# Optimization experiments

Measured on AMD Instinct MI355X. Metric: run time of the kernel, lower is better.

The kernel has to match this reference:

```python
import jax, jax.numpy as jnp
import numpy as np

T = 200                      # TRAIN_ROIS_PER_IMAGE
RATIO = 0.33                 # ROI_POSITIVE_RATIO
P_MAX = int(T * RATIO)       # max positive ROIs (66)
MH, MW = 28, 28              # MASK_SHAPE
STD = jnp.array([0.1, 0.1, 0.2, 0.2], jnp.float32)  # BBOX_STD_DEV
EPS = 1e-6


def _iou(a, b):
    # a [N,4], b [G,4] -> [N,G] IoU (same math as overlaps_graph, without tiling)
    ay1, ax1, ay2, ax2 = a[:, 0:1], a[:, 1:2], a[:, 2:3], a[:, 3:4]
    by1, bx1, by2, bx2 = b[None, :, 0], b[None, :, 1], b[None, :, 2], b[None, :, 3]
    iy = jnp.maximum(jnp.minimum(ay2, by2) - jnp.maximum(ay1, by1), 0.0)
    ix = jnp.maximum(jnp.minimum(ax2, bx2) - jnp.maximum(ax1, bx1), 0.0)
    inter = iy * ix
    union = (ay2 - ay1) * (ax2 - ax1) + (by2 - by1) * (bx2 - bx1) - inter
    return inter / jnp.maximum(union, EPS)


def _box_refinement(box, gt):
    # standard Mask R-CNN box_refinement_graph
    h = jnp.maximum(box[:, 2] - box[:, 0], EPS)
    w = jnp.maximum(box[:, 3] - box[:, 1], EPS)
    cy = box[:, 0] + 0.5 * h
    cx = box[:, 1] + 0.5 * w
    gh = jnp.maximum(gt[:, 2] - gt[:, 0], EPS)
    gw = jnp.maximum(gt[:, 3] - gt[:, 1], EPS)
    gcy = gt[:, 0] + 0.5 * gh
    gcx = gt[:, 1] + 0.5 * gw
    return jnp.stack([(gcy - cy) / h, (gcx - cx) / w,
                      jnp.log(gh / h), jnp.log(gw / w)], axis=-1)


def _crop_and_resize(imgs, boxes):
    # imgs [T,H,W], boxes [T,4] normalized; TF crop_and_resize bilinear semantics,
    # extrapolation_value = 0 for samples outside [0, H-1] x [0, W-1].
    Tn, H, W = imgs.shape
    y1, x1, y2, x2 = boxes[:, 0], boxes[:, 1], boxes[:, 2], boxes[:, 3]
    iy = jnp.arange(MH, dtype=jnp.float32)
    ix = jnp.arange(MW, dtype=jnp.float32)
    ys = y1[:, None] * (H - 1) + iy[None, :] * ((y2 - y1) * (H - 1) / (MH - 1))[:, None]  # [T,MH]
    xs = x1[:, None] * (W - 1) + ix[None, :] * ((x2 - x1) * (W - 1) / (MW - 1))[:, None]  # [T,MW]
    y0 = jnp.floor(ys); x0 = jnp.floor(xs)
    wy = (ys - y0)[:, :, None]
    wx = (xs - x0)[:, None, :]
    y0i = jnp.clip(y0, 0, H - 1).astype(jnp.int32)
    y1i = jnp.clip(y0 + 1, 0, H - 1).astype(jnp.int32)
    x0i = jnp.clip(x0, 0, W - 1).astype(jnp.int32)
    x1i = jnp.clip(x0 + 1, 0, W - 1).astype(jnp.int32)
    t = jnp.arange(Tn)[:, None, None]
    v00 = imgs[t, y0i[:, :, None], x0i[:, None, :]]
    v01 = imgs[t, y0i[:, :, None], x1i[:, None, :]]
    v10 = imgs[t, y1i[:, :, None], x0i[:, None, :]]
    v11 = imgs[t, y1i[:, :, None], x1i[:, None, :]]
    val = (v00 * (1 - wx) + v01 * wx) * (1 - wy) + (v10 * (1 - wx) + v11 * wx) * wy
    ok = ((ys >= 0) & (ys <= H - 1))[:, :, None] & ((xs >= 0) & (xs <= W - 1))[:, None, :]
    return jnp.where(ok, val, 0.0)


def _targets_one(proposals, class_ids, boxes, masks):
    # proposals [N,4], class_ids [G] int, boxes [G,4], masks [H,W,G]
    N = proposals.shape[0]
    # zero-padding trim expressed as validity masks (jit-friendly fixed shapes)
    valid_prop = jnp.any(proposals != 0, axis=1)
    valid_gt = jnp.any(boxes != 0, axis=1)
    non_crowd = (class_ids > 0) & valid_gt
    crowd = (class_ids < 0) & valid_gt

    ov = _iou(proposals, boxes)                              # [N,G]
    ov_nc = jnp.where(non_crowd[None, :], ov, -1.0)          # mask crowd/padded gt
    roi_iou_max = ov_nc.max(axis=1)
    crowd_max = jnp.where(crowd[None, :], ov, 0.0).max(axis=1)

    pos_mask = valid_prop & (roi_iou_max >= 0.5)
    neg_mask = valid_prop & (roi_iou_max < 0.5) & (crowd_max < 0.001)

    # deterministic selection (original uses tf.random.shuffle): positives first-in-order
    pos_order = jnp.argsort(jnp.where(pos_mask, 0, 1))
    neg_order = jnp.argsort(jnp.where(neg_mask, 0, 1))
    pos_count = jnp.minimum(pos_mask.sum(), P_MAX)
    neg_needed = jnp.floor(pos_count.astype(jnp.float32) / RATIO).astype(jnp.int32) - pos_count
    neg_count = jnp.minimum(jnp.minimum(neg_needed, neg_mask.sum()), T - pos_count)

    slot = jnp.arange(T)
    is_pos = slot < pos_count
    is_neg = (slot >= pos_count) & (slot < pos_count + neg_count)
    src = jnp.where(is_pos,
                    pos_order[jnp.clip(slot, 0, N - 1)],
                    neg_order[jnp.clip(slot - pos_count, 0, N - 1)])
    rois = jnp.where((is_pos | is_neg)[:, None], proposals[src], 0.0)

    assign = jnp.argmax(ov_nc[src], axis=1)                  # gt assignment per slot
    gt_box = boxes[assign]
    gt_cls = jnp.where(is_pos, class_ids[assign], 0)

    deltas = _box_refinement(rois, gt_box) / STD
    deltas = jnp.where(is_pos[:, None], deltas, 0.0)

    # USE_MINI_MASK: roi box in gt-box-normalized coordinates
    gy1, gx1, gy2, gx2 = gt_box[:, 0], gt_box[:, 1], gt_box[:, 2], gt_box[:, 3]
    gh = jnp.maximum(gy2 - gy1, EPS)
    gw = jnp.maximum(gx2 - gx1, EPS)
    mm = jnp.stack([(rois[:, 0] - gy1) / gh, (rois[:, 1] - gx1) / gw,
                    (rois[:, 2] - gy1) / gh, (rois[:, 3] - gx1) / gw], axis=-1)

    roi_masks = jnp.moveaxis(jnp.take(masks, assign, axis=2), 2, 0)  # [T,H,W]
    m = jnp.round(_crop_and_resize(roi_masks, mm))
    m = jnp.where(is_pos[:, None, None], m, 0.0)
    return rois, gt_cls, deltas, m


def setup_inputs() -> dict:
    key = jax.random.key(0)
    ks = jax.random.split(key, 4)
    B, N, G, HM = 16, 2000, 200, 56

    def boxes_of(k, shape):
        k1, k2, k3, k4 = jax.random.split(k, 4)
        y1 = jax.random.uniform(k1, shape) * 0.5
        x1 = jax.random.uniform(k2, shape) * 0.5
        h = 0.1 + jax.random.uniform(k3, shape) * 0.4
        w = 0.1 + jax.random.uniform(k4, shape) * 0.4
        return jnp.stack([y1, x1, y1 + h, x1 + w], axis=-1)

    proposals = boxes_of(ks[0], (B, N))
    proposals = proposals * (jnp.arange(N) < N - 200)[None, :, None]  # zero-padded tail
    prior_class_ids = jax.random.randint(ks[1], (B, G), -1, 81).astype(jnp.int32)  # -1=crowd, 0=padding
    prior_boxes = boxes_of(ks[2], (B, G)) * (prior_class_ids != 0)[..., None]
    prior_masks = (jax.random.uniform(ks[3], (B, HM, HM, G)) > 0.5).astype(jnp.float32)
    return {"proposals": proposals, "prior_class_ids": prior_class_ids,
            "prior_boxes": prior_boxes, "prior_masks": prior_masks}


def reference(proposals, prior_class_ids, prior_boxes, prior_masks):
    rois, cls, deltas, masks = jax.vmap(_targets_one)(proposals, prior_class_ids,
                                                      prior_boxes, prior_masks)
    return rois, cls, deltas, masks
```

## Files before the change

### kernel.cpp

```cpp
#include <hip/hip_runtime.h>
#include <math.h>

#pragma clang fp contract(off)

#define BN     16
#define NP     2000
#define NG     200
#define NT     200
#define PMAX   66
#define EPSF   1e-6f
#define MH     28
#define MW     28
#define HM     56
#define NPIX   (HM*HM)
#define NPLANE 66

__global__ __launch_bounds__(256) void kA(
    const float* __restrict__ proposals, const int* __restrict__ cls_ids,
    const float* __restrict__ boxes,
    int* __restrict__ flag_ws, int* __restrict__ assign_ws)
{
#pragma clang fp contract(off)
  const int b = blockIdx.y;
  __shared__ float4 gbox[NG];
  __shared__ float  garea[NG];
  __shared__ int    gflag[NG];

  for (int j = threadIdx.x; j < NG; j += 256) {
    float4 g = reinterpret_cast<const float4*>(boxes + (size_t)b * NG * 4)[j];
    int c = cls_ids[b * NG + j];
    bool vg = (g.x != 0.f) || (g.y != 0.f) || (g.z != 0.f) || (g.w != 0.f);
    gbox[j]  = g;
    garea[j] = (g.z - g.x) * (g.w - g.y);
    gflag[j] = vg ? (c > 0 ? 1 : (c < 0 ? 2 : 0)) : 0;
  }
  __syncthreads();

  int i = blockIdx.x * 256 + threadIdx.x;
  if (i >= NP) return;

  float4 p = reinterpret_cast<const float4*>(proposals + (size_t)b * NP * 4)[i];
  bool vp = (p.x != 0.f) || (p.y != 0.f) || (p.z != 0.f) || (p.w != 0.f);
  if (!vp) {
    flag_ws[b * NP + i] = 0;
    assign_ws[b * NP + i] = 0;
    return;
  }
  float pa = (p.z - p.x) * (p.w - p.y);

  float best = -3.0e38f;
  int   bestj = 0;
  float cmax = 0.f;
  for (int j = 0; j < NG; ++j) {
    float4 g = gbox[j];
    float iy = fmaxf(fminf(p.z, g.z) - fmaxf(p.x, g.x), 0.f);
    float ix = fmaxf(fminf(p.w, g.w) - fmaxf(p.y, g.y), 0.f);
    float inter = iy * ix;
    float uni = (pa + garea[j]) - inter;
    float iou = inter / fmaxf(uni, EPSF);
    int fl = gflag[j];
    float v = (fl == 1) ? iou : -1.0f;
    if (v > best) { best = v; bestj = j; }
    if (fl == 2) cmax = fmaxf(cmax, iou);
  }
  bool pos = (best >= 0.5f);
  bool neg = (best < 0.5f) && (cmax < 0.001f);
  flag_ws[b * NP + i]   = pos ? 1 : (neg ? 2 : 0);
  assign_ws[b * NP + i] = bestj;
}

__global__ __launch_bounds__(256) void kB(
    const float* __restrict__ proposals, const int* __restrict__ cls_ids,
    const float* __restrict__ boxes, const int* __restrict__ flag_ws,
    const int* __restrict__ assign_ws, float* __restrict__ out,
    float* __restrict__ mm_ws, int* __restrict__ pa_ws,
    int* __restrict__ gmap_ws, int* __restrict__ ucount_ws)
{
#pragma clang fp contract(off)
  const int b = blockIdx.x;
  const int tid = threadIdx.x;
  const int lane = tid & 63;
  const int wv = tid >> 6;

  __shared__ unsigned short pos_list[NP];
  __shared__ unsigned short neg_list[NP];
  __shared__ int wcp[4], wcn[4];
  __shared__ int s_pt, s_nt;
  __shared__ int used[NG];
  __shared__ int gplane[NG];
  __shared__ int wtot[4];
  if (tid == 0) { s_pt = 0; s_nt = 0; }
  __syncthreads();

  const int* fb = flag_ws + b * NP;
  for (int base = 0; base < NP; base += 256) {
    int i = base + tid;
    int f = (i < NP) ? fb[i] : 0;
    bool isp = (f == 1), isn = (f == 2);
    unsigned long long bp = __ballot(isp);
    unsigned long long bn = __ballot(isn);
    __syncthreads();
    if (lane == 0) { wcp[wv] = __popcll(bp); wcn[wv] = __popcll(bn); }
    __syncthreads();
    int prep = __popcll(bp & ((1ull << lane) - 1ull));
    int pren = __popcll(bn & ((1ull << lane) - 1ull));
    int bpp = 0, bnn = 0, tp = 0, tn = 0;
    for (int w = 0; w < 4; ++w) {
      if (w < wv) { bpp += wcp[w]; bnn += wcn[w]; }
      tp += wcp[w]; tn += wcn[w];
    }
    int pt = s_pt, nt = s_nt;
    if (isp) pos_list[pt + bpp + prep] = (unsigned short)i;
    if (isn) neg_list[nt + bnn + pren] = (unsigned short)i;
    __syncthreads();
    if (tid == 0) { s_pt = pt + tp; s_nt = nt + tn; }
  }
  __syncthreads();

  int pos_total = s_pt, neg_total = s_nt;
  int pos_count = min(pos_total, PMAX);
  int neg_needed = (int)floorf((float)pos_count / 0.33f) - pos_count;
  int neg_count = min(min(neg_needed, neg_total), NT - pos_count);

  for (int j = tid; j < NG; j += 256) used[j] = 0;
  __syncthreads();

  int ma = -1;
  if (tid < NT) {
    bool ispos = tid < pos_count;
    bool isneg = (!ispos) && (tid < pos_count + neg_count);
    float r0 = 0.f, r1 = 0.f, r2 = 0.f, r3 = 0.f;
    float d0 = 0.f, d1 = 0.f, d2 = 0.f, d3 = 0.f;
    float m0 = 0.f, m1 = 0.f, m2 = 0.f, m3 = 0.f;
    float clsf = 0.f;
    if (ispos || isneg) {
      int i = ispos ? (int)pos_list[tid] : (int)neg_list[tid - pos_count];
      float4 p = reinterpret_cast<const float4*>(proposals + (size_t)b * NP * 4)[i];
      r0 = p.x; r1 = p.y; r2 = p.z; r3 = p.w;
      if (ispos) {
        int a = assign_ws[b * NP + i];
        ma = a;
        used[a] = 1;
        float4 g = reinterpret_cast<const float4*>(boxes + (size_t)b * NG * 4)[a];
        float h  = fmaxf(r2 - r0, EPSF);
        float w  = fmaxf(r3 - r1, EPSF);
        float cy = r0 + 0.5f * h;
        float cx = r1 + 0.5f * w;
        float gh = fmaxf(g.z - g.x, EPSF);
        float gw = fmaxf(g.w - g.y, EPSF);
        float gcy = g.x + 0.5f * gh;
        float gcx = g.y + 0.5f * gw;
        d0 = ((gcy - cy) / h) / 0.1f;
        d1 = ((gcx - cx) / w) / 0.1f;
        d2 = logf(gh / h) / 0.2f;
        d3 = logf(gw / w) / 0.2f;
        m0 = (r0 - g.x) / gh;
        m1 = (r1 - g.y) / gw;
        m2 = (r2 - g.x) / gh;
        m3 = (r3 - g.y) / gw;
        clsf = (float)cls_ids[b * NG + a];
      }
    }
    int s = b * NT + tid;
    float* rois = out;
    float* cls  = out + BN * NT * 4;
    float* dlt  = out + BN * NT * 4 + BN * NT;
    rois[s * 4 + 0] = r0; rois[s * 4 + 1] = r1;
    rois[s * 4 + 2] = r2; rois[s * 4 + 3] = r3;
    cls[s] = clsf;
    dlt[s * 4 + 0] = d0; dlt[s * 4 + 1] = d1;
    dlt[s * 4 + 2] = d2; dlt[s * 4 + 3] = d3;
    mm_ws[s * 4 + 0] = m0; mm_ws[s * 4 + 1] = m1;
    mm_ws[s * 4 + 2] = m2; mm_ws[s * 4 + 3] = m3;
  }
  __syncthreads();

  {
    int j = tid;
    int u = (j < NG) ? used[j] : 0;
    unsigned long long m = __ballot(u != 0);
    int pre = __popcll(m & ((1ull << lane) - 1ull));
    if (lane == 0) wtot[wv] = __popcll(m);
    __syncthreads();
    int basep = 0;
    for (int w = 0; w < wv; ++w) basep += wtot[w];
    if (j < NG) {
      int pl = u ? (basep + pre) : -1;
      gplane[j] = pl;
      gmap_ws[b * NG + j] = pl;
    }
  }
  __syncthreads();

  if (tid == 0)
    ucount_ws[b] = wtot[0] + wtot[1] + wtot[2] + wtot[3];
  if (tid < NT)
    pa_ws[b * NT + tid] = (ma >= 0) ? gplane[ma] : -1;
}

__global__ __launch_bounds__(256) void kG(
    const float* __restrict__ masks, const int* __restrict__ gmap_ws,
    const int* __restrict__ ucount_ws, float* __restrict__ staged)
{
  const int b   = blockIdx.y;
  const int p0  = blockIdx.x * 64;
  const int tid = threadIdx.x;
  const int lane = tid & 63;
  const int wv   = tid >> 6;

  __shared__ float tile[64][204];
  __shared__ unsigned short glist[NG];

  if (tid < NG) {
    int pl = gmap_ws[b * NG + tid];
    if (pl >= 0) glist[pl] = (unsigned short)tid;
  }
  const int U = ucount_ws[b];

  const float* mb = masks + (size_t)b * NPIX * NG;
  for (int r = 0; r < 16; ++r) {
    int pl = r * 4 + wv;
    if (lane < 50) {
      float4 v = *reinterpret_cast<const float4*>(
          mb + (size_t)(p0 + pl) * NG + lane * 4);
      *reinterpret_cast<float4*>(&tile[pl][lane * 4]) = v;
    }
  }
  __syncthreads();

  for (int u = wv; u < U; u += 4) {
    int g = (int)glist[u];
    staged[(size_t)(b * NPLANE + u) * NPIX + p0 + lane] = tile[lane][g];
  }
}

__global__ __launch_bounds__(256) void kC(
    const float* __restrict__ staged, const float* __restrict__ mm_ws,
    const int* __restrict__ pa_ws, float* __restrict__ out)
{
#pragma clang fp contract(off)
  const int s = blockIdx.x;
  float4* om = reinterpret_cast<float4*>(
      out + (size_t)(BN * NT * 9) + (size_t)s * (MH * MW));
  const int q = threadIdx.x;
  if (q >= (MH * MW) / 4) return;
  int pa = pa_ws[s];
  if (pa < 0) { om[q] = make_float4(0.f, 0.f, 0.f, 0.f); return; }

  const int b = s / NT;
  float y1 = mm_ws[s * 4 + 0], x1 = mm_ws[s * 4 + 1];
  float y2 = mm_ws[s * 4 + 2], x2 = mm_ws[s * 4 + 3];
  float sy = (y2 - y1) * 55.0f / 27.0f;
  float sx = (x2 - x1) * 55.0f / 27.0f;
  const float* mp = staged + (size_t)(b * NPLANE + pa) * NPIX;

  int px0 = q * 4;
  int my  = px0 / MW;
  float ys = y1 * 55.0f + (float)my * sy;
  float y0f = floorf(ys);
  float wy  = ys - y0f;
  int y0i = (int)fminf(fmaxf(y0f, 0.f), 55.f);
  int y1i = (int)fminf(fmaxf(y0f + 1.0f, 0.f), 55.f);
  bool oky = (ys >= 0.f) && (ys <= 55.f);
  const float* r0 = mp + y0i * HM;
  const float* r1 = mp + y1i * HM;

  float res[4];
  for (int k = 0; k < 4; ++k) {
    int mx = (px0 + k) - my * MW;
    float xs = x1 * 55.0f + (float)mx * sx;
    float x0f = floorf(xs);
    float wx  = xs - x0f;
    int x0i = (int)fminf(fmaxf(x0f, 0.f), 55.f);
    int x1i = (int)fminf(fmaxf(x0f + 1.0f, 0.f), 55.f);
    float v00 = r0[x0i], v01 = r0[x1i];
    float v10 = r1[x0i], v11 = r1[x1i];
    float val = (v00 * (1.f - wx) + v01 * wx) * (1.f - wy)
              + (v10 * (1.f - wx) + v11 * wx) * wy;
    bool ok = oky && (xs >= 0.f) && (xs <= 55.f);
    res[k] = ok ? rintf(val) : 0.f;
  }
  om[q] = make_float4(res[0], res[1], res[2], res[3]);
}

extern "C" void kernel_launch(void* const* d_in, const int* in_sizes, int n_in,
                              void* d_out, int out_size, void* d_ws, size_t ws_size,
                              hipStream_t stream)
{
  const float* proposals = (const float*)d_in[0];
  const int*   cls_ids   = (const int*)d_in[1];
  const float* boxes     = (const float*)d_in[2];
  const float* masks     = (const float*)d_in[3];
  float* out = (float*)d_out;

  char* ws = (char*)d_ws;
  int*   flag_ws   = (int*)ws;    ws += (size_t)BN * NP * sizeof(int);
  int*   assign_ws = (int*)ws;    ws += (size_t)BN * NP * sizeof(int);
  float* mm_ws     = (float*)ws;  ws += (size_t)BN * NT * 4 * sizeof(float);
  int*   pa_ws     = (int*)ws;    ws += (size_t)BN * NT * sizeof(int);
  int*   gmap_ws   = (int*)ws;    ws += (size_t)BN * NG * sizeof(int);
  int*   ucount_ws = (int*)ws;    ws += (size_t)BN * sizeof(int);
  float* staged    = (float*)ws;

  dim3 gA((NP + 255) / 256, BN);
  kA<<<gA, 256, 0, stream>>>(proposals, cls_ids, boxes, flag_ws, assign_ws);
  kB<<<BN, 256, 0, stream>>>(proposals, cls_ids, boxes, flag_ws, assign_ws,
                             out, mm_ws, pa_ws, gmap_ws, ucount_ws);
  dim3 gG(NPIX / 64, BN);
  kG<<<gG, 256, 0, stream>>>(masks, gmap_ws, ucount_ws, staged);
  kC<<<BN * NT, 256, 0, stream>>>(staged, mm_ws, pa_ws, out);
}
```

Baseline: 130.1 us.

## Fuse four kernels into one cooperative persistent kernel with grid syncs

Replaces the four separate launches (IoU matching, sampling, mask gather, crop-resize) with one cooperative kernel of 256 blocks that uses grid-wide syncs between stages. Shared memory is pooled into one buffer reused by each stage, and the gather and resize stages become grid-stride loops. The aim is to remove per-launch overhead and inter-kernel gaps. In exchange it adds grid-barrier cost, and stages with little work (the 16-block sampling stage) leave most blocks idle while they wait.

Result: slower. 282.1 us (+116.9%).

```diff
diff --git a/kernel.cpp b/kernel.cpp
--- a/kernel.cpp
+++ b/kernel.cpp
@@ -1,7 +1,10 @@
 #include <hip/hip_runtime.h>
+#include <hip/hip_cooperative_groups.h>
 #include <math.h>
 
 #pragma clang fp contract(off)
+
+namespace cg = cooperative_groups;
 
 #define BN     16
 #define NP     2000
@@ -14,273 +17,277 @@
 #define HM     56
 #define NPIX   (HM*HM)
 #define NPLANE 66
-
-__global__ __launch_bounds__(256) void kA(
+#define NBLK   256
+
+#define SMEM_BYTES 52640
+
+__global__ __launch_bounds__(256) void kFused(
     const float* __restrict__ proposals, const int* __restrict__ cls_ids,
-    const float* __restrict__ boxes,
-    int* __restrict__ flag_ws, int* __restrict__ assign_ws)
+    const float* __restrict__ boxes, const float* __restrict__ masks,
+    float* __restrict__ out,
+    int* __restrict__ flag_ws, int* __restrict__ assign_ws,
+    float* __restrict__ mm_ws, int* __restrict__ pa_ws,
+    int* __restrict__ gmap_ws, int* __restrict__ ucount_ws,
+    float* __restrict__ staged)
 {
 #pragma clang fp contract(off)
-  const int b = blockIdx.y;
-  __shared__ float4 gbox[NG];
-  __shared__ float  garea[NG];
-  __shared__ int    gflag[NG];
-
-  for (int j = threadIdx.x; j < NG; j += 256) {
-    float4 g = reinterpret_cast<const float4*>(boxes + (size_t)b * NG * 4)[j];
-    int c = cls_ids[b * NG + j];
-    bool vg = (g.x != 0.f) || (g.y != 0.f) || (g.z != 0.f) || (g.w != 0.f);
-    gbox[j]  = g;
-    garea[j] = (g.z - g.x) * (g.w - g.y);
-    gflag[j] = vg ? (c > 0 ? 1 : (c < 0 ? 2 : 0)) : 0;
-  }
-  __syncthreads();
-
-  int i = blockIdx.x * 256 + threadIdx.x;
-  if (i >= NP) return;
-
-  float4 p = reinterpret_cast<const float4*>(proposals + (size_t)b * NP * 4)[i];
-  bool vp = (p.x != 0.f) || (p.y != 0.f) || (p.z != 0.f) || (p.w != 0.f);
-  if (!vp) {
-    flag_ws[b * NP + i] = 0;
-    assign_ws[b * NP + i] = 0;
-    return;
-  }
-  float pa = (p.z - p.x) * (p.w - p.y);
-
-  float best = -3.0e38f;
-  int   bestj = 0;
-  float cmax = 0.f;
-  for (int j = 0; j < NG; ++j) {
-    float4 g = gbox[j];
-    float iy = fmaxf(fminf(p.z, g.z) - fmaxf(p.x, g.x), 0.f);
-    float ix = fmaxf(fminf(p.w, g.w) - fmaxf(p.y, g.y), 0.f);
-    float inter = iy * ix;
-    float uni = (pa + garea[j]) - inter;
-    float iou = inter / fmaxf(uni, EPSF);
-    int fl = gflag[j];
-    float v = (fl == 1) ? iou : -1.0f;
-    if (v > best) { best = v; bestj = j; }
-    if (fl == 2) cmax = fmaxf(cmax, iou);
-  }
-  bool pos = (best >= 0.5f);
-  bool neg = (best < 0.5f) && (cmax < 0.001f);
-  flag_ws[b * NP + i]   = pos ? 1 : (neg ? 2 : 0);
-  assign_ws[b * NP + i] = bestj;
-}
-
-__global__ __launch_bounds__(256) void kB(
-    const float* __restrict__ proposals, const int* __restrict__ cls_ids,
-    const float* __restrict__ boxes, const int* __restrict__ flag_ws,
-    const int* __restrict__ assign_ws, float* __restrict__ out,
-    float* __restrict__ mm_ws, int* __restrict__ pa_ws,
-    int* __restrict__ gmap_ws, int* __restrict__ ucount_ws)
-{
-#pragma clang fp contract(off)
-  const int b = blockIdx.x;
-  const int tid = threadIdx.x;
-  const int lane = tid & 63;
-  const int wv = tid >> 6;
-
-  __shared__ unsigned short pos_list[NP];
-  __shared__ unsigned short neg_list[NP];
-  __shared__ int wcp[4], wcn[4];
+  __shared__ __align__(16) char smem[SMEM_BYTES];
+  __shared__ int wcp[4], wcn[4], wtot[4];
   __shared__ int s_pt, s_nt;
-  __shared__ int used[NG];
-  __shared__ int gplane[NG];
-  __shared__ int wtot[4];
-  if (tid == 0) { s_pt = 0; s_nt = 0; }
-  __syncthreads();
-
-  const int* fb = flag_ws + b * NP;
-  for (int base = 0; base < NP; base += 256) {
-    int i = base + tid;
-    int f = (i < NP) ? fb[i] : 0;
-    bool isp = (f == 1), isn = (f == 2);
-    unsigned long long bp = __ballot(isp);
-    unsigned long long bn = __ballot(isn);
-    __syncthreads();
-    if (lane == 0) { wcp[wv] = __popcll(bp); wcn[wv] = __popcll(bn); }
-    __syncthreads();
-    int prep = __popcll(bp & ((1ull << lane) - 1ull));
-    int pren = __popcll(bn & ((1ull << lane) - 1ull));
-    int bpp = 0, bnn = 0, tp = 0, tn = 0;
-    for (int w = 0; w < 4; ++w) {
-      if (w < wv) { bpp += wcp[w]; bnn += wcn[w]; }
-      tp += wcp[w]; tn += wcn[w];
-    }
-    int pt = s_pt, nt = s_nt;
-    if (isp) pos_list[pt + bpp + prep] = (unsigned short)i;
-    if (isn) neg_list[nt + bnn + pren] = (unsigned short)i;
-    __syncthreads();
-    if (tid == 0) { s_pt = pt + tp; s_nt = nt + tn; }
-  }
-  __syncthreads();
-
-  int pos_total = s_pt, neg_total = s_nt;
-  int pos_count = min(pos_total, PMAX);
-  int neg_needed = (int)floorf((float)pos_count / 0.33f) - pos_count;
-  int neg_count = min(min(neg_needed, neg_total), NT - pos_count);
-
-  for (int j = tid; j < NG; j += 256) used[j] = 0;
-  __syncthreads();
-
-  int ma = -1;
-  if (tid < NT) {
-    bool ispos = tid < pos_count;
-    bool isneg = (!ispos) && (tid < pos_count + neg_count);
-    float r0 = 0.f, r1 = 0.f, r2 = 0.f, r3 = 0.f;
-    float d0 = 0.f, d1 = 0.f, d2 = 0.f, d3 = 0.f;
-    float m0 = 0.f, m1 = 0.f, m2 = 0.f, m3 = 0.f;
-    float clsf = 0.f;
-    if (ispos || isneg) {
-      int i = ispos ? (int)pos_list[tid] : (int)neg_list[tid - pos_count];
-      float4 p = reinterpret_cast<const float4*>(proposals + (size_t)b * NP * 4)[i];
-      r0 = p.x; r1 = p.y; r2 = p.z; r3 = p.w;
-      if (ispos) {
-        int a = assign_ws[b * NP + i];
-        ma = a;
-        used[a] = 1;
-        float4 g = reinterpret_cast<const float4*>(boxes + (size_t)b * NG * 4)[a];
-        float h  = fmaxf(r2 - r0, EPSF);
-        float w  = fmaxf(r3 - r1, EPSF);
-        float cy = r0 + 0.5f * h;
-        float cx = r1 + 0.5f * w;
-        float gh = fmaxf(g.z - g.x, EPSF);
-        float gw = fmaxf(g.w - g.y, EPSF);
-        float gcy = g.x + 0.5f * gh;
-        float gcx = g.y + 0.5f * gw;
-        d0 = ((gcy - cy) / h) / 0.1f;
-        d1 = ((gcx - cx) / w) / 0.1f;
-        d2 = logf(gh / h) / 0.2f;
-        d3 = logf(gw / w) / 0.2f;
-        m0 = (r0 - g.x) / gh;
-        m1 = (r1 - g.y) / gw;
-        m2 = (r2 - g.x) / gh;
-        m3 = (r3 - g.y) / gw;
-        clsf = (float)cls_ids[b * NG + a];
-      }
-    }
-    int s = b * NT + tid;
-    float* rois = out;
-    float* cls  = out + BN * NT * 4;
-    float* dlt  = out + BN * NT * 4 + BN * NT;
-    rois[s * 4 + 0] = r0; rois[s * 4 + 1] = r1;
-    rois[s * 4 + 2] = r2; rois[s * 4 + 3] = r3;
-    cls[s] = clsf;
-    dlt[s * 4 + 0] = d0; dlt[s * 4 + 1] = d1;
-    dlt[s * 4 + 2] = d2; dlt[s * 4 + 3] = d3;
-    mm_ws[s * 4 + 0] = m0; mm_ws[s * 4 + 1] = m1;
-    mm_ws[s * 4 + 2] = m2; mm_ws[s * 4 + 3] = m3;
-  }
-  __syncthreads();
-
-  {
-    int j = tid;
-    int u = (j < NG) ? used[j] : 0;
-    unsigned long long m = __ballot(u != 0);
-    int pre = __popcll(m & ((1ull << lane) - 1ull));
-    if (lane == 0) wtot[wv] = __popcll(m);
-    __syncthreads();
-    int basep = 0;
-    for (int w = 0; w < wv; ++w) basep += wtot[w];
-    if (j < NG) {
-      int pl = u ? (basep + pre) : -1;
-      gplane[j] = pl;
-      gmap_ws[b * NG + j] = pl;
-    }
-  }
-  __syncthreads();
-
-  if (tid == 0)
-    ucount_ws[b] = wtot[0] + wtot[1] + wtot[2] + wtot[3];
-  if (tid < NT)
-    pa_ws[b * NT + tid] = (ma >= 0) ? gplane[ma] : -1;
-}
-
-__global__ __launch_bounds__(256) void kG(
-    const float* __restrict__ masks, const int* __restrict__ gmap_ws,
-    const int* __restrict__ ucount_ws, float* __restrict__ staged)
-{
-  const int b   = blockIdx.y;
-  const int p0  = blockIdx.x * 64;
-  const int tid = threadIdx.x;
+
+  cg::grid_group grid = cg::this_grid();
+  const int tid  = threadIdx.x;
   const int lane = tid & 63;
   const int wv   = tid >> 6;
-
-  __shared__ float tile[64][204];
-  __shared__ unsigned short glist[NG];
-
-  if (tid < NG) {
-    int pl = gmap_ws[b * NG + tid];
-    if (pl >= 0) glist[pl] = (unsigned short)tid;
+  const int blk  = blockIdx.x;
+
+  if (blk < BN * 8) {
+    const int b     = blk >> 3;
+    const int chunk = blk & 7;
+    float4* gbox = (float4*)smem;
+    float*  garea = (float*)(smem + 3200);
+    int*    gflag = (int*)(smem + 4000);
+
+    if (tid < NG) {
+      float4 g = reinterpret_cast<const float4*>(boxes + (size_t)b * NG * 4)[tid];
+      int c = cls_ids[b * NG + tid];
+      bool vg = (g.x != 0.f) || (g.y != 0.f) || (g.z != 0.f) || (g.w != 0.f);
+      gbox[tid]  = g;
+      garea[tid] = (g.z - g.x) * (g.w - g.y);
+      gflag[tid] = vg ? (c > 0 ? 1 : (c < 0 ? 2 : 0)) : 0;
+    }
+    __syncthreads();
+
+    int i = chunk * 256 + tid;
+    if (i < NP) {
+      float4 p = reinterpret_cast<const float4*>(proposals + (size_t)b * NP * 4)[i];
+      bool vp = (p.x != 0.f) || (p.y != 0.f) || (p.z != 0.f) || (p.w != 0.f);
+      if (!vp) {
+        flag_ws[b * NP + i]   = 0;
+        assign_ws[b * NP + i] = 0;
+      } else {
+        float pa = (p.z - p.x) * (p.w - p.y);
+        float best = -3.0e38f;
+        int   bestj = 0;
+        float cmax = 0.f;
+        for (int j = 0; j < NG; ++j) {
+          float4 g = gbox[j];
+          float iy = fmaxf(fminf(p.z, g.z) - fmaxf(p.x, g.x), 0.f);
+          float ix = fmaxf(fminf(p.w, g.w) - fmaxf(p.y, g.y), 0.f);
+          float inter = iy * ix;
+          float uni = (pa + garea[j]) - inter;
+          float iou = inter / fmaxf(uni, EPSF);
+          int fl = gflag[j];
+          float v = (fl == 1) ? iou : -1.0f;
+          if (v > best) { best = v; bestj = j; }
+          if (fl == 2) cmax = fmaxf(cmax, iou);
+        }
+        bool pos = (best >= 0.5f);
+        bool neg = (best < 0.5f) && (cmax < 0.001f);
+        flag_ws[b * NP + i]   = pos ? 1 : (neg ? 2 : 0);
+        assign_ws[b * NP + i] = bestj;
+      }
+    }
   }
-  const int U = ucount_ws[b];
-
-  const float* mb = masks + (size_t)b * NPIX * NG;
-  for (int r = 0; r < 16; ++r) {
-    int pl = r * 4 + wv;
-    if (lane < 50) {
-      float4 v = *reinterpret_cast<const float4*>(
-          mb + (size_t)(p0 + pl) * NG + lane * 4);
-      *reinterpret_cast<float4*>(&tile[pl][lane * 4]) = v;
-    }
+  __threadfence();
+  grid.sync();
+
+  if (blk < BN) {
+    const int b = blk;
+    unsigned short* pos_list = (unsigned short*)smem;
+    unsigned short* neg_list = (unsigned short*)(smem + 4000);
+    int* used   = (int*)(smem + 8000);
+    int* gplane = (int*)(smem + 8800);
+
+    if (tid == 0) { s_pt = 0; s_nt = 0; }
+    __syncthreads();
+
+    const int* fb = flag_ws + b * NP;
+    for (int base = 0; base < NP; base += 256) {
+      int i = base + tid;
+      int f = (i < NP) ? fb[i] : 0;
+      bool isp = (f == 1), isn = (f == 2);
+      unsigned long long bp = __ballot(isp);
+      unsigned long long bn = __ballot(isn);
+      __syncthreads();
+      if (lane == 0) { wcp[wv] = __popcll(bp); wcn[wv] = __popcll(bn); }
+      __syncthreads();
+      int prep = __popcll(bp & ((1ull << lane) - 1ull));
+      int pren = __popcll(bn & ((1ull << lane) - 1ull));
+      int bpp = 0, bnn = 0, tp = 0, tn = 0;
+      for (int w = 0; w < 4; ++w) {
+        if (w < wv) { bpp += wcp[w]; bnn += wcn[w]; }
+        tp += wcp[w]; tn += wcn[w];
+      }
+      int pt = s_pt, nt = s_nt;
+      if (isp) pos_list[pt + bpp + prep] = (unsigned short)i;
+      if (isn) neg_list[nt + bnn + pren] = (unsigned short)i;
+      __syncthreads();
+      if (tid == 0) { s_pt = pt + tp; s_nt = nt + tn; }
+    }
+    __syncthreads();
+
+    int pos_total = s_pt, neg_total = s_nt;
+    int pos_count = min(pos_total, PMAX);
+    int neg_needed = (int)floorf((float)pos_count / 0.33f) - pos_count;
+    int neg_count = min(min(neg_needed, neg_total), NT - pos_count);
+
+    if (tid < NG) used[tid] = 0;
+    __syncthreads();
+
+    int ma = -1;
+    if (tid < NT) {
+      bool ispos = tid < pos_count;
+      bool isneg = (!ispos) && (tid < pos_count + neg_count);
+      float r0 = 0.f, r1 = 0.f, r2 = 0.f, r3 = 0.f;
+      float d0 = 0.f, d1 = 0.f, d2 = 0.f, d3 = 0.f;
+      float m0 = 0.f, m1 = 0.f, m2 = 0.f, m3 = 0.f;
+      float clsf = 0.f;
+      if (ispos || isneg) {
+        int i = ispos ? (int)pos_list[tid] : (int)neg_list[tid - pos_count];
+        float4 p = reinterpret_cast<const float4*>(proposals + (size_t)b * NP * 4)[i];
+        r0 = p.x; r1 = p.y; r2 = p.z; r3 = p.w;
+        if (ispos) {
+          int a = assign_ws[b * NP + i];
+          ma = a;
+          used[a] = 1;
+          float4 g = reinterpret_cast<const float4*>(boxes + (size_t)b * NG * 4)[a];
+          float h  = fmaxf(r2 - r0, EPSF);
+          float w  = fmaxf(r3 - r1, EPSF);
+          float cy = r0 + 0.5f * h;
+          float cx = r1 + 0.5f * w;
+          float gh = fmaxf(g.z - g.x, EPSF);
+          float gw = fmaxf(g.w - g.y, EPSF);
+          float gcy = g.x + 0.5f * gh;
+          float gcx = g.y + 0.5f * gw;
+          d0 = ((gcy - cy) / h) / 0.1f;
+          d1 = ((gcx - cx) / w) / 0.1f;
+          d2 = logf(gh / h) / 0.2f;
+          d3 = logf(gw / w) / 0.2f;
+          m0 = (r0 - g.x) / gh;
+          m1 = (r1 - g.y) / gw;
+          m2 = (r2 - g.x) / gh;
+          m3 = (r3 - g.y) / gw;
+          clsf = (float)cls_ids[b * NG + a];
+        }
+      }
+      int s = b * NT + tid;
+      float* rois = out;
+      float* cls  = out + BN * NT * 4;
+      float* dlt  = out + BN * NT * 4 + BN * NT;
+      rois[s * 4 + 0] = r0; rois[s * 4 + 1] = r1;
+      rois[s * 4 + 2] = r2; rois[s * 4 + 3] = r3;
+      cls[s] = clsf;
+      dlt[s * 4 + 0] = d0; dlt[s * 4 + 1] = d1;
+      dlt[s * 4 + 2] = d2; dlt[s * 4 + 3] = d3;
+      mm_ws[s * 4 + 0] = m0; mm_ws[s * 4 + 1] = m1;
+      mm_ws[s * 4 + 2] = m2; mm_ws[s * 4 + 3] = m3;
+    }
+    __syncthreads();
+
+    {
+      int j = tid;
+      int u = (j < NG) ? used[j] : 0;
+      unsigned long long m = __ballot(u != 0);
+      int pre = __popcll(m & ((1ull << lane) - 1ull));
+      if (lane == 0) wtot[wv] = __popcll(m);
+      __syncthreads();
+      int basep = 0;
+      for (int w = 0; w < wv; ++w) basep += wtot[w];
+      if (j < NG) {
+        int pl = u ? (basep + pre) : -1;
+        gplane[j] = pl;
+        gmap_ws[b * NG + j] = pl;
+      }
+    }
+    __syncthreads();
+
+    if (tid == 0)
+      ucount_ws[b] = wtot[0] + wtot[1] + wtot[2] + wtot[3];
+    if (tid < NT)
+      pa_ws[b * NT + tid] = (ma >= 0) ? gplane[ma] : -1;
   }
-  __syncthreads();
-
-  for (int u = wv; u < U; u += 4) {
-    int g = (int)glist[u];
-    staged[(size_t)(b * NPLANE + u) * NPIX + p0 + lane] = tile[lane][g];
+  __threadfence();
+  grid.sync();
+
+  {
+    float (*tile)[204] = (float(*)[204])smem;
+    unsigned short* glist = (unsigned short*)(smem + 52224);
+
+    for (int u = blk; u < BN * 49; u += NBLK) {
+      int b  = u / 49;
+      int p0 = (u - b * 49) * 64;
+      __syncthreads();
+      if (tid < NG) {
+        int pl = gmap_ws[b * NG + tid];
+        if (pl >= 0) glist[pl] = (unsigned short)tid;
+      }
+      const int U = ucount_ws[b];
+
+      const float* mb = masks + (size_t)b * NPIX * NG;
+      for (int r = 0; r < 16; ++r) {
+        int pl = r * 4 + wv;
+        if (lane < 50) {
+          float4 v = *reinterpret_cast<const float4*>(
+              mb + (size_t)(p0 + pl) * NG + lane * 4);
+          *reinterpret_cast<float4*>(&tile[pl][lane * 4]) = v;
+        }
+      }
+      __syncthreads();
+      for (int u2 = wv; u2 < U; u2 += 4) {
+        int g = (int)glist[u2];
+        staged[(size_t)(b * NPLANE + u2) * NPIX + p0 + lane] = tile[lane][g];
+      }
+    }
   }
-}
-
-__global__ __launch_bounds__(256) void kC(
-    const float* __restrict__ staged, const float* __restrict__ mm_ws,
-    const int* __restrict__ pa_ws, float* __restrict__ out)
-{
-#pragma clang fp contract(off)
-  const int s = blockIdx.x;
-  float4* om = reinterpret_cast<float4*>(
-      out + (size_t)(BN * NT * 9) + (size_t)s * (MH * MW));
-  const int q = threadIdx.x;
-  if (q >= (MH * MW) / 4) return;
-  int pa = pa_ws[s];
-  if (pa < 0) { om[q] = make_float4(0.f, 0.f, 0.f, 0.f); return; }
-
-  const int b = s / NT;
-  float y1 = mm_ws[s * 4 + 0], x1 = mm_ws[s * 4 + 1];
-  float y2 = mm_ws[s * 4 + 2], x2 = mm_ws[s * 4 + 3];
-  float sy = (y2 - y1) * 55.0f / 27.0f;
-  float sx = (x2 - x1) * 55.0f / 27.0f;
-  const float* mp = staged + (size_t)(b * NPLANE + pa) * NPIX;
-
-  int px0 = q * 4;
-  int my  = px0 / MW;
-  float ys = y1 * 55.0f + (float)my * sy;
-  float y0f = floorf(ys);
-  float wy  = ys - y0f;
-  int y0i = (int)fminf(fmaxf(y0f, 0.f), 55.f);
-  int y1i = (int)fminf(fmaxf(y0f + 1.0f, 0.f), 55.f);
-  bool oky = (ys >= 0.f) && (ys <= 55.f);
-  const float* r0 = mp + y0i * HM;
-  const float* r1 = mp + y1i * HM;
-
-  float res[4];
-  for (int k = 0; k < 4; ++k) {
-    int mx = (px0 + k) - my * MW;
-    float xs = x1 * 55.0f + (float)mx * sx;
-    float x0f = floorf(xs);
-    float wx  = xs - x0f;
-    int x0i = (int)fminf(fmaxf(x0f, 0.f), 55.f);
-    int x1i = (int)fminf(fmaxf(x0f + 1.0f, 0.f), 55.f);
-    float v00 = r0[x0i], v01 = r0[x1i];
-    float v10 = r1[x0i], v11 = r1[x1i];
-    float val = (v00 * (1.f - wx) + v01 * wx) * (1.f - wy)
-              + (v10 * (1.f - wx) + v11 * wx) * wy;
-    bool ok = oky && (xs >= 0.f) && (xs <= 55.f);
-    res[k] = ok ? rintf(val) : 0.f;
+  __threadfence();
+  grid.sync();
+
+  {
+    const int q = tid;
+    for (int s = blk; s < BN * NT; s += NBLK) {
+      if (q >= (MH * MW) / 4) continue;
+      float4* om = reinterpret_cast<float4*>(
+          out + (size_t)(BN * NT * 9) + (size_t)s * (MH * MW));
+      int pa = pa_ws[s];
+      if (pa < 0) { om[q] = make_float4(0.f, 0.f, 0.f, 0.f); continue; }
+
+      const int b = s / NT;
+      float y1 = mm_ws[s * 4 + 0], x1 = mm_ws[s * 4 + 1];
+      float y2 = mm_ws[s * 4 + 2], x2 = mm_ws[s * 4 + 3];
+      float sy = (y2 - y1) * 55.0f / 27.0f;
+      float sx = (x2 - x1) * 55.0f / 27.0f;
+      const float* mp = staged + (size_t)(b * NPLANE + pa) * NPIX;
+
+      int px0 = q * 4;
+      int my  = px0 / MW;
+      float ys = y1 * 55.0f + (float)my * sy;
+      float y0f = floorf(ys);
+      float wy  = ys - y0f;
+      int y0i = (int)fminf(fmaxf(y0f, 0.f), 55.f);
+      int y1i = (int)fminf(fmaxf(y0f + 1.0f, 0.f), 55.f);
+      bool oky = (ys >= 0.f) && (ys <= 55.f);
+      const float* r0 = mp + y0i * HM;
+      const float* r1 = mp + y1i * HM;
+
+      float res[4];
+      for (int k = 0; k < 4; ++k) {
+        int mx = (px0 + k) - my * MW;
+        float xs = x1 * 55.0f + (float)mx * sx;
+        float x0f = floorf(xs);
+        float wx  = xs - x0f;
+        int x0i = (int)fminf(fmaxf(x0f, 0.f), 55.f);
+        int x1i = (int)fminf(fmaxf(x0f + 1.0f, 0.f), 55.f);
+        float v00 = r0[x0i], v01 = r0[x1i];
+        float v10 = r1[x0i], v11 = r1[x1i];
+        float val = (v00 * (1.f - wx) + v01 * wx) * (1.f - wy)
+                  + (v10 * (1.f - wx) + v11 * wx) * wy;
+        bool ok = oky && (xs >= 0.f) && (xs <= 55.f);
+        res[k] = ok ? rintf(val) : 0.f;
+      }
+      om[q] = make_float4(res[0], res[1], res[2], res[3]);
+    }
   }
-  om[q] = make_float4(res[0], res[1], res[2], res[3]);
 }
 
 extern "C" void kernel_launch(void* const* d_in, const int* in_sizes, int n_in,
@@ -302,11 +309,11 @@
   int*   ucount_ws = (int*)ws;    ws += (size_t)BN * sizeof(int);
   float* staged    = (float*)ws;
 
-  dim3 gA((NP + 255) / 256, BN);
-  kA<<<gA, 256, 0, stream>>>(proposals, cls_ids, boxes, flag_ws, assign_ws);
-  kB<<<BN, 256, 0, stream>>>(proposals, cls_ids, boxes, flag_ws, assign_ws,
-                             out, mm_ws, pa_ws, gmap_ws, ucount_ws);
-  dim3 gG(NPIX / 64, BN);
-  kG<<<gG, 256, 0, stream>>>(masks, gmap_ws, ucount_ws, staged);
-  kC<<<BN * NT, 256, 0, stream>>>(staged, mm_ws, pa_ws, out);
+  void* args[] = {
+    (void*)&proposals, (void*)&cls_ids, (void*)&boxes, (void*)&masks,
+    (void*)&out, (void*)&flag_ws, (void*)&assign_ws, (void*)&mm_ws,
+    (void*)&pa_ws, (void*)&gmap_ws, (void*)&ucount_ws, (void*)&staged
+  };
+  hipLaunchCooperativeKernel((const void*)kFused, dim3(NBLK), dim3(256),
+                             args, 0, stream);
 }
```
